# Kernel optimization log

Hardware: AMD Instinct MI355X
Metric: run time of the kernel (lower is better)

The kernel has to match this reference:

```python
import jax, jax.numpy as jnp
import numpy as np

B, V, J, NB = 512, 6890, 24, 10
P = (J - 1) * 9  # 207 pose-blendshape features

# Standard SMPL kinematic tree (root parent = -1)
SMPL_PARENTS = np.array([-1, 0, 0, 0, 1, 2, 3, 4, 5, 6, 7, 8, 9, 9, 9,
                         12, 13, 14, 16, 17, 18, 19, 20, 21], dtype=np.int32)


def setup_inputs() -> dict:
    key = jax.random.key(0)
    ks = jax.random.split(key, 7)
    betas = jax.random.normal(ks[0], (B, NB), jnp.float32)
    pose = 0.2 * jax.random.normal(ks[1], (B, J * 3), jnp.float32)
    v_template = jax.random.normal(ks[2], (V, 3), jnp.float32)
    shapedirs = 0.01 * jax.random.normal(ks[3], (V, 3, NB), jnp.float32)
    posedirs = 0.01 * jax.random.normal(ks[4], (P, V * 3), jnp.float32)
    J_regressor = jax.random.uniform(ks[5], (J, V), jnp.float32)
    J_regressor = J_regressor / jnp.sum(J_regressor, axis=1, keepdims=True)
    lbs_weights = jax.random.uniform(ks[6], (V, J), jnp.float32)
    lbs_weights = lbs_weights / jnp.sum(lbs_weights, axis=1, keepdims=True)
    parents = jnp.asarray(SMPL_PARENTS)
    return {"betas": betas, "pose": pose, "v_template": v_template,
            "shapedirs": shapedirs, "posedirs": posedirs,
            "J_regressor": J_regressor, "lbs_weights": lbs_weights,
            "parents": parents}


def batch_rodrigues(aa):
    """Axis-angle (N,3) -> rotation matrices (N,3,3), matching the torch impl."""
    angle = jnp.linalg.norm(aa + 1e-8, axis=1, keepdims=True)  # (N,1)
    rd = aa / angle
    cos = jnp.cos(angle)[:, :, None]  # (N,1,1)
    sin = jnp.sin(angle)[:, :, None]
    rx, ry, rz = rd[:, 0], rd[:, 1], rd[:, 2]
    zeros = jnp.zeros_like(rx)
    K = jnp.stack([zeros, -rz, ry,
                   rz, zeros, -rx,
                   -ry, rx, zeros], axis=1).reshape(-1, 3, 3)
    ident = jnp.eye(3, dtype=aa.dtype)
    return ident + sin * K + (1.0 - cos) * jnp.matmul(K, K)


def reference(betas, pose, v_template, shapedirs, posedirs, J_regressor,
              lbs_weights, parents):
    par = np.asarray(parents)  # static kinematic tree (host constants)
    b = betas.shape[0]
    nj = J_regressor.shape[0]
    # shape blendshapes: v_shaped = v_template + sum_l betas_l * shapedirs[...,l]
    v_shaped = v_template[None] + jnp.einsum('bl,vkl->bvk', betas, shapedirs)
    Jloc = jnp.einsum('bvk,jv->bjk', v_shaped, J_regressor)  # (b,J,3)
    rot = batch_rodrigues(pose.reshape(-1, 3)).reshape(b, nj, 3, 3)
    # pose blendshapes
    ident = jnp.eye(3, dtype=rot.dtype)
    pose_feature = (rot[:, 1:] - ident).reshape(b, -1)  # (b,207)
    v_posed = v_shaped + (pose_feature @ posedirs).reshape(b, -1, 3)
    # relative joint locations
    rel = Jloc.at[:, 1:].add(-Jloc[:, par[1:]])
    # per-joint local transforms (b,J,4,4)
    top = jnp.concatenate([rot, rel[..., None]], axis=-1)  # (b,J,3,4)
    bottom = jnp.broadcast_to(jnp.array([0., 0., 0., 1.], dtype=rot.dtype),
                              (b, nj, 1, 4))
    tm = jnp.concatenate([top, bottom], axis=2)
    # kinematic chain (fixed, tiny loop over 24 joints with static parents)
    chain = [tm[:, 0]]
    for i in range(1, par.shape[0]):
        chain.append(chain[par[i]] @ tm[:, i])
    transforms = jnp.stack(chain, axis=1)  # (b,J,4,4) absolute transforms
    posed_joints = transforms[:, :, :3, 3]
    # remove rest-pose joint offset: A = transforms - [0|transforms @ [J;0]]
    jh = jnp.concatenate([Jloc, jnp.zeros_like(Jloc[..., :1])], axis=-1)
    init_bone = jnp.einsum('bjpq,bjq->bjp', transforms, jh)  # (b,J,4)
    A = transforms - jnp.pad(init_bone[..., None], ((0, 0), (0, 0), (0, 0), (3, 0)))
    # linear blend skinning: per-vertex transform T = sum_j w_vj * A_j
    T = jnp.einsum('vj,bjpq->bvpq', lbs_weights, A)  # (b,V,4,4)
    verts = jnp.einsum('bvpk,bvk->bvp', T[:, :, :3, :3], v_posed) + T[:, :, :3, 3]
    return verts, posed_joints, A, transforms, v_posed
```

## Files before the change

kernel.cpp:

```cpp
#include <hip/hip_runtime.h>
#include <hip/hip_bf16.h>

#define BB 512
#define VV 6890
#define NJ 24
#define NBETA 10
#define NP 207
#define N3 (VV*3)
#define TBAT 16

#define OFF_VERTS 0
#define OFF_PJ   (BB*VV*3)
#define OFF_A    (OFF_PJ + BB*NJ*3)
#define OFF_TF   (OFF_A + BB*NJ*16)
#define OFF_VP   (OFF_TF + BB*NJ*16)

#define WS_JTJS 0
#define WS_PF   (WS_JTJS + NJ*33)
#define WS_A    (WS_PF + BB*NP)

__constant__ int c_par[NJ] = {-1, 0, 0, 0, 1, 2, 3, 4, 5, 6, 7, 8,
                              9, 9, 9, 12, 13, 14, 16, 17, 18, 19, 20, 21};

__global__ void k_jreg(const float* __restrict__ jr,
                       const float* __restrict__ vt,
                       const float* __restrict__ sd,
                       float* __restrict__ ws) {
    int j = blockIdx.x / 33, idx = blockIdx.x % 33;
    int t = threadIdx.x;
    float acc = 0.f;
    for (int v = t; v < VV; v += 256) {
        float a = jr[j * VV + v];
        float x = (idx < 3) ? vt[v * 3 + idx] : sd[v * 30 + (idx - 3)];
        acc += a * x;
    }
    __shared__ float red[256];
    red[t] = acc;
    __syncthreads();
    for (int s = 128; s > 0; s >>= 1) {
        if (t < s) red[t] += red[t + s];
        __syncthreads();
    }
    if (t == 0) ws[WS_JTJS + j * 33 + idx] = red[0];
}

__global__ __launch_bounds__(64) void k_chain(
        const float* __restrict__ betas,
        const float* __restrict__ pose,
        const float* __restrict__ ws_jtjs,
        float* __restrict__ ws_pf,
        float* __restrict__ ws_A,
        float* __restrict__ out) {
    int b = blockIdx.x;
    int t = threadIdx.x;
    __shared__ float Jl[NJ][3];
    __shared__ float tm[NJ][16];
    __shared__ float ch[NJ][16];
    float R[9];

    if (t < NJ) {
        int j = t;
        float bb[NBETA];
#pragma unroll
        for (int l = 0; l < NBETA; l++) bb[l] = betas[b * NBETA + l];
#pragma unroll
        for (int k = 0; k < 3; k++) {
            float acc = ws_jtjs[j * 33 + k];
#pragma unroll
            for (int l = 0; l < NBETA; l++) acc += bb[l] * ws_jtjs[j * 33 + 3 + k * NBETA + l];
            Jl[j][k] = acc;
        }
        float ax = pose[b * NJ * 3 + j * 3 + 0];
        float ay = pose[b * NJ * 3 + j * 3 + 1];
        float az = pose[b * NJ * 3 + j * 3 + 2];
        float e0 = ax + 1e-8f, e1 = ay + 1e-8f, e2 = az + 1e-8f;
        float ang = sqrtf(e0 * e0 + e1 * e1 + e2 * e2);
        float inv = 1.f / ang;
        float rx = ax * inv, ry = ay * inv, rz = az * inv;
        float sn = sinf(ang), cs = cosf(ang);
        float Km[9] = {0.f, -rz, ry, rz, 0.f, -rx, -ry, rx, 0.f};
#pragma unroll
        for (int r = 0; r < 3; r++)
#pragma unroll
            for (int c = 0; c < 3; c++) {
                float kk = Km[3 * r + 0] * Km[0 + c] + Km[3 * r + 1] * Km[3 + c] +
                           Km[3 * r + 2] * Km[6 + c];
                R[3 * r + c] = ((r == c) ? 1.f : 0.f) + sn * Km[3 * r + c] + (1.f - cs) * kk;
            }
        if (j >= 1) {
#pragma unroll
            for (int e = 0; e < 9; e++) {
                int r = e / 3, c = e % 3;
                ws_pf[b * NP + (j - 1) * 9 + e] = R[e] - ((r == c) ? 1.f : 0.f);
            }
        }
    }
    __syncthreads();
    if (t < NJ) {
        int j = t;
        int p = c_par[j];
        int ps = (p < 0) ? 0 : p;
#pragma unroll
        for (int r = 0; r < 3; r++) {
            tm[j][r * 4 + 0] = R[3 * r + 0];
            tm[j][r * 4 + 1] = R[3 * r + 1];
            tm[j][r * 4 + 2] = R[3 * r + 2];
            tm[j][r * 4 + 3] = (j == 0) ? Jl[j][r] : (Jl[j][r] - Jl[ps][r]);
        }
        tm[j][12] = 0.f; tm[j][13] = 0.f; tm[j][14] = 0.f; tm[j][15] = 1.f;
    }
    __syncthreads();
    if (t < 16) ch[0][t] = tm[0][t];
    __syncthreads();
    for (int i = 1; i < NJ; i++) {
        if (t < 16) {
            int r = t >> 2, c = t & 3;
            int p = c_par[i];
            ch[i][t] = ch[p][4 * r + 0] * tm[i][0 + c] + ch[p][4 * r + 1] * tm[i][4 + c] +
                       ch[p][4 * r + 2] * tm[i][8 + c] + ch[p][4 * r + 3] * tm[i][12 + c];
        }
        __syncthreads();
    }
    if (t < NJ) {
        int j = t;
        float ib[4];
#pragma unroll
        for (int p = 0; p < 4; p++)
            ib[p] = ch[j][4 * p + 0] * Jl[j][0] + ch[j][4 * p + 1] * Jl[j][1] +
                    ch[j][4 * p + 2] * Jl[j][2];
#pragma unroll
        for (int e = 0; e < 16; e++) {
            int r = e >> 2, c = e & 3;
            float tr = ch[j][e];
            float Ae = tr - ((c == 3) ? ib[r] : 0.f);
            out[OFF_TF + (size_t)(b * NJ + j) * 16 + e] = tr;
            out[OFF_A + (size_t)(b * NJ + j) * 16 + e] = Ae;
            ws_A[(size_t)(b * NJ + j) * 16 + e] = Ae;
        }
#pragma unroll
        for (int k = 0; k < 3; k++)
            out[OFF_PJ + (size_t)(b * NJ + j) * 3 + k] = ch[j][4 * k + 3];
    }
}

__global__ __launch_bounds__(256, 4) void k_posed(
        const float* __restrict__ vt,
        const float* __restrict__ sd,
        const float* __restrict__ betas,
        const float* __restrict__ pd,
        const float* __restrict__ ws_pf,
        float* __restrict__ out) {
    int b0 = blockIdx.y * TBAT;
    int n0 = (blockIdx.x * 256 + threadIdx.x) * 2;
    if (n0 >= N3) return;

    float acc0[TBAT], acc1[TBAT];
#pragma unroll
    for (int bi = 0; bi < TBAT; bi++) { acc0[bi] = 0.f; acc1[bi] = 0.f; }

    for (int p0 = 0; p0 < NP; p0 += 9) {
        float pdv0[9], pdv1[9];
#pragma unroll
        for (int pc = 0; pc < 9; pc++) {
            const float2 v = *(const float2*)&pd[(size_t)(p0 + pc) * N3 + n0];
            pdv0[pc] = v.x; pdv1[pc] = v.y;
        }
#pragma unroll
        for (int bi = 0; bi < TBAT; bi++) {
            const float* __restrict__ pfr = &ws_pf[(size_t)(b0 + bi) * NP + p0];
#pragma unroll
            for (int pc = 0; pc < 9; pc++) {
                float w = pfr[pc];
                acc0[bi] += w * pdv0[pc];
                acc1[bi] += w * pdv1[pc];
            }
        }
    }

    float base0 = vt[n0], base1 = vt[n0 + 1];
    float sdv0[NBETA], sdv1[NBETA];
#pragma unroll
    for (int l = 0; l < NBETA; l++) {
        sdv0[l] = sd[(size_t)n0 * NBETA + l];
        sdv1[l] = sd[(size_t)(n0 + 1) * NBETA + l];
    }
#pragma unroll
    for (int bi = 0; bi < TBAT; bi++) {
        const float* __restrict__ br = &betas[(size_t)(b0 + bi) * NBETA];
        float s0 = base0 + acc0[bi], s1 = base1 + acc1[bi];
#pragma unroll
        for (int l = 0; l < NBETA; l++) {
            float bl = br[l];
            s0 += bl * sdv0[l];
            s1 += bl * sdv1[l];
        }
        float2 o; o.x = s0; o.y = s1;
        *(float2*)&out[OFF_VP + (size_t)(b0 + bi) * N3 + n0] = o;
    }
}

__global__ void k_verts(const float* __restrict__ lw,
                        const float* __restrict__ ws_A,
                        float* __restrict__ out) {
    int b = blockIdx.y;
    int v = blockIdx.x * 256 + threadIdx.x;
    if (v >= VV) return;

    float wv[NJ];
#pragma unroll
    for (int j0 = 0; j0 < NJ; j0 += 4) {
        const float4 w4 = *(const float4*)&lw[(size_t)v * NJ + j0];
        wv[j0 + 0] = w4.x; wv[j0 + 1] = w4.y; wv[j0 + 2] = w4.z; wv[j0 + 3] = w4.w;
    }

    float T[12];
#pragma unroll
    for (int e = 0; e < 12; e++) T[e] = 0.f;
    const float* __restrict__ Ab = ws_A + (size_t)b * NJ * 16;
#pragma unroll
    for (int j = 0; j < NJ; j++) {
        const float* __restrict__ Aj = Ab + j * 16;
        float wj = wv[j];
#pragma unroll
        for (int e = 0; e < 12; e++) T[e] += wj * Aj[e];
    }

    size_t base = (size_t)(b * VV + v) * 3;
    float x = out[OFF_VP + base + 0];
    float y = out[OFF_VP + base + 1];
    float z = out[OFF_VP + base + 2];
#pragma unroll
    for (int p = 0; p < 3; p++) {
        out[OFF_VERTS + base + p] =
            T[4 * p + 0] * x + T[4 * p + 1] * y + T[4 * p + 2] * z + T[4 * p + 3];
    }
}

extern "C" void kernel_launch(void* const* d_in, const int* in_sizes, int n_in,
                              void* d_out, int out_size, void* d_ws, size_t ws_size,
                              hipStream_t stream) {
    const float* betas = (const float*)d_in[0];
    const float* pose  = (const float*)d_in[1];
    const float* vt    = (const float*)d_in[2];
    const float* sd    = (const float*)d_in[3];
    const float* pd    = (const float*)d_in[4];
    const float* jr    = (const float*)d_in[5];
    const float* lw    = (const float*)d_in[6];
    float* out = (float*)d_out;
    float* ws = (float*)d_ws;

    k_jreg<<<NJ * 33, 256, 0, stream>>>(jr, vt, sd, ws);
    k_chain<<<BB, 64, 0, stream>>>(betas, pose, ws + WS_JTJS, ws + WS_PF,
                                   ws + WS_A, out);
    k_posed<<<dim3((N3 / 2 + 255) / 256, BB / TBAT), 256, 0, stream>>>(
        vt, sd, betas, pd, ws + WS_PF, out);
    k_verts<<<dim3((VV + 255) / 256, BB), 256, 0, stream>>>(lw, ws + WS_A, out);
}
```

Baseline: 231.0 us.

## Restructure jreg, posed, and verts kernels with chunking, XCD swizzle, and batching

After: 255.4 us. 1.11x slower.

```diff
diff --git a/kernel.cpp b/kernel.cpp
--- a/kernel.cpp
+++ b/kernel.cpp
@@ -7,7 +7,10 @@
 #define NBETA 10
 #define NP 207
 #define N3 (VV*3)
-#define TBAT 16
+#define TBAT 8
+#define NCH 16
+#define CHV ((VV + NCH - 1) / NCH)
+#define VB 4
 
 #define OFF_VERTS 0
 #define OFF_PJ   (BB*VV*3)
@@ -15,39 +18,58 @@
 #define OFF_TF   (OFF_A + BB*NJ*16)
 #define OFF_VP   (OFF_TF + BB*NJ*16)
 
-#define WS_JTJS 0
-#define WS_PF   (WS_JTJS + NJ*33)
+#define WS_JP   0
+#define WS_PF   (WS_JP + NCH*NJ*33)
 #define WS_A    (WS_PF + BB*NP)
 
 __constant__ int c_par[NJ] = {-1, 0, 0, 0, 1, 2, 3, 4, 5, 6, 7, 8,
                               9, 9, 9, 12, 13, 14, 16, 17, 18, 19, 20, 21};
 
-__global__ void k_jreg(const float* __restrict__ jr,
-                       const float* __restrict__ vt,
-                       const float* __restrict__ sd,
-                       float* __restrict__ ws) {
-    int j = blockIdx.x / 33, idx = blockIdx.x % 33;
+__global__ __launch_bounds__(256) void k_jreg(const float* __restrict__ jr,
+                                              const float* __restrict__ vt,
+                                              const float* __restrict__ sd,
+                                              float* __restrict__ ws_jp) {
+    int j = blockIdx.x, ch = blockIdx.y;
     int t = threadIdx.x;
-    float acc = 0.f;
-    for (int v = t; v < VV; v += 256) {
-        float a = jr[j * VV + v];
-        float x = (idx < 3) ? vt[v * 3 + idx] : sd[v * 30 + (idx - 3)];
-        acc += a * x;
-    }
-    __shared__ float red[256];
-    red[t] = acc;
+    int v0 = ch * CHV;
+    int vend = (v0 + CHV < VV) ? (v0 + CHV) : VV;
+
+    float acc[33];
+#pragma unroll
+    for (int i = 0; i < 33; i++) acc[i] = 0.f;
+
+    for (int v = v0 + t; v < vend; v += 256) {
+        float a = jr[(size_t)j * VV + v];
+        acc[0] += a * vt[v * 3 + 0];
+        acc[1] += a * vt[v * 3 + 1];
+        acc[2] += a * vt[v * 3 + 2];
+        const float2* sp = (const float2*)&sd[(size_t)v * 30];
+#pragma unroll
+        for (int i = 0; i < 15; i++) {
+            float2 s = sp[i];
+            acc[3 + 2 * i] += a * s.x;
+            acc[4 + 2 * i] += a * s.y;
+        }
+    }
+
+    __shared__ float red[33][256];
+#pragma unroll
+    for (int i = 0; i < 33; i++) red[i][t] = acc[i];
     __syncthreads();
     for (int s = 128; s > 0; s >>= 1) {
-        if (t < s) red[t] += red[t + s];
+        if (t < s) {
+#pragma unroll
+            for (int i = 0; i < 33; i++) red[i][t] += red[i][t + s];
+        }
         __syncthreads();
     }
-    if (t == 0) ws[WS_JTJS + j * 33 + idx] = red[0];
+    if (t < 33) ws_jp[(size_t)(ch * NJ + j) * 33 + t] = red[t][0];
 }
 
 __global__ __launch_bounds__(64) void k_chain(
         const float* __restrict__ betas,
         const float* __restrict__ pose,
-        const float* __restrict__ ws_jtjs,
+        const float* __restrict__ ws_jp,
         float* __restrict__ ws_pf,
         float* __restrict__ ws_A,
         float* __restrict__ out) {
@@ -60,14 +82,22 @@
 
     if (t < NJ) {
         int j = t;
+        float s[33];
+#pragma unroll
+        for (int i = 0; i < 33; i++) s[i] = 0.f;
+        for (int c = 0; c < NCH; c++) {
+            const float* pp = ws_jp + (size_t)(c * NJ + j) * 33;
+#pragma unroll
+            for (int i = 0; i < 33; i++) s[i] += pp[i];
+        }
         float bb[NBETA];
 #pragma unroll
         for (int l = 0; l < NBETA; l++) bb[l] = betas[b * NBETA + l];
 #pragma unroll
         for (int k = 0; k < 3; k++) {
-            float acc = ws_jtjs[j * 33 + k];
-#pragma unroll
-            for (int l = 0; l < NBETA; l++) acc += bb[l] * ws_jtjs[j * 33 + 3 + k * NBETA + l];
+            float acc = s[k];
+#pragma unroll
+            for (int l = 0; l < NBETA; l++) acc += bb[l] * s[3 + k * NBETA + l];
             Jl[j][k] = acc;
         }
         float ax = pose[b * NJ * 3 + j * 3 + 0];
@@ -143,6 +173,29 @@
     }
 }
 
+__device__ __forceinline__ void load9(const float* __restrict__ pdp, int c0,
+                                      float* b0, float* b1) {
+#pragma unroll
+    for (int pc = 0; pc < 9; pc++) {
+        float2 v = *(const float2*)&pdp[(size_t)(c0 + pc) * N3];
+        b0[pc] = v.x; b1[pc] = v.y;
+    }
+}
+__device__ __forceinline__ void comp9(const float* __restrict__ ws_pf, int b0, int c0,
+                                      const float* pv0, const float* pv1,
+                                      float* acc0, float* acc1) {
+#pragma unroll
+    for (int bi = 0; bi < TBAT; bi++) {
+        const float* __restrict__ pfr = &ws_pf[(size_t)(b0 + bi) * NP + c0];
+#pragma unroll
+        for (int pc = 0; pc < 9; pc++) {
+            float w = pfr[pc];
+            acc0[bi] += w * pv0[pc];
+            acc1[bi] += w * pv1[pc];
+        }
+    }
+}
+
 __global__ __launch_bounds__(256, 4) void k_posed(
         const float* __restrict__ vt,
         const float* __restrict__ sd,
@@ -150,32 +203,33 @@
         const float* __restrict__ pd,
         const float* __restrict__ ws_pf,
         float* __restrict__ out) {
-    int b0 = blockIdx.y * TBAT;
-    int n0 = (blockIdx.x * 256 + threadIdx.x) * 2;
+    int id = blockIdx.x;
+    int xcd = id & 7, li = id >> 3;
+    int nx = (xcd == 0) ? 6 : 5;
+    if (li >= nx * (BB / TBAT)) return;
+    int x = xcd + 8 * (li % nx);
+    int y = li / nx;
+    int b0 = y * TBAT;
+    int n0 = (x * 256 + threadIdx.x) * 2;
     if (n0 >= N3) return;
 
     float acc0[TBAT], acc1[TBAT];
 #pragma unroll
     for (int bi = 0; bi < TBAT; bi++) { acc0[bi] = 0.f; acc1[bi] = 0.f; }
 
-    for (int p0 = 0; p0 < NP; p0 += 9) {
-        float pdv0[9], pdv1[9];
-#pragma unroll
-        for (int pc = 0; pc < 9; pc++) {
-            const float2 v = *(const float2*)&pd[(size_t)(p0 + pc) * N3 + n0];
-            pdv0[pc] = v.x; pdv1[pc] = v.y;
-        }
-#pragma unroll
-        for (int bi = 0; bi < TBAT; bi++) {
-            const float* __restrict__ pfr = &ws_pf[(size_t)(b0 + bi) * NP + p0];
-#pragma unroll
-            for (int pc = 0; pc < 9; pc++) {
-                float w = pfr[pc];
-                acc0[bi] += w * pdv0[pc];
-                acc1[bi] += w * pdv1[pc];
-            }
-        }
-    }
+    float pA0[9], pA1[9], pB0[9], pB1[9];
+    const float* __restrict__ pdp = pd + n0;
+
+    load9(pdp, 0, pA0, pA1);
+#pragma unroll 1
+    for (int c = 0; c < 11; c++) {
+        int c0 = c * 18;
+        load9(pdp, c0 + 9, pB0, pB1);
+        comp9(ws_pf, b0, c0, pA0, pA1, acc0, acc1);
+        load9(pdp, c0 + 18, pA0, pA1);
+        comp9(ws_pf, b0, c0 + 9, pB0, pB1, acc0, acc1);
+    }
+    comp9(ws_pf, b0, 198, pA0, pA1, acc0, acc1);
 
     float base0 = vt[n0], base1 = vt[n0 + 1];
     float sdv0[NBETA], sdv1[NBETA];
@@ -199,10 +253,10 @@
     }
 }
 
-__global__ void k_verts(const float* __restrict__ lw,
-                        const float* __restrict__ ws_A,
-                        float* __restrict__ out) {
-    int b = blockIdx.y;
+__global__ __launch_bounds__(256, 4) void k_verts(const float* __restrict__ lw,
+                                                  const float* __restrict__ ws_A,
+                                                  float* __restrict__ out) {
+    int bq = blockIdx.y;
     int v = blockIdx.x * 256 + threadIdx.x;
     if (v >= VV) return;
 
@@ -213,26 +267,29 @@
         wv[j0 + 0] = w4.x; wv[j0 + 1] = w4.y; wv[j0 + 2] = w4.z; wv[j0 + 3] = w4.w;
     }
 
-    float T[12];
-#pragma unroll
-    for (int e = 0; e < 12; e++) T[e] = 0.f;
-    const float* __restrict__ Ab = ws_A + (size_t)b * NJ * 16;
-#pragma unroll
-    for (int j = 0; j < NJ; j++) {
-        const float* __restrict__ Aj = Ab + j * 16;
-        float wj = wv[j];
-#pragma unroll
-        for (int e = 0; e < 12; e++) T[e] += wj * Aj[e];
-    }
-
-    size_t base = (size_t)(b * VV + v) * 3;
-    float x = out[OFF_VP + base + 0];
-    float y = out[OFF_VP + base + 1];
-    float z = out[OFF_VP + base + 2];
-#pragma unroll
-    for (int p = 0; p < 3; p++) {
-        out[OFF_VERTS + base + p] =
-            T[4 * p + 0] * x + T[4 * p + 1] * y + T[4 * p + 2] * z + T[4 * p + 3];
+#pragma unroll
+    for (int bb = 0; bb < VB; bb++) {
+        int b = bq * VB + bb;
+        const float* __restrict__ Ab = ws_A + (size_t)b * NJ * 16;
+        float T[12];
+#pragma unroll
+        for (int e = 0; e < 12; e++) T[e] = 0.f;
+#pragma unroll
+        for (int j = 0; j < NJ; j++) {
+            const float* __restrict__ Aj = Ab + j * 16;
+            float wj = wv[j];
+#pragma unroll
+            for (int e = 0; e < 12; e++) T[e] += wj * Aj[e];
+        }
+        size_t base = (size_t)(b * VV + v) * 3;
+        float xx = out[OFF_VP + base + 0];
+        float yy = out[OFF_VP + base + 1];
+        float zz = out[OFF_VP + base + 2];
+#pragma unroll
+        for (int p = 0; p < 3; p++) {
+            out[OFF_VERTS + base + p] =
+                T[4 * p + 0] * xx + T[4 * p + 1] * yy + T[4 * p + 2] * zz + T[4 * p + 3];
+        }
     }
 }
 
@@ -249,10 +306,10 @@
     float* out = (float*)d_out;
     float* ws = (float*)d_ws;
 
-    k_jreg<<<NJ * 33, 256, 0, stream>>>(jr, vt, sd, ws);
-    k_chain<<<BB, 64, 0, stream>>>(betas, pose, ws + WS_JTJS, ws + WS_PF,
+    k_jreg<<<dim3(NJ, NCH), 256, 0, stream>>>(jr, vt, sd, ws + WS_JP);
+    k_chain<<<BB, 64, 0, stream>>>(betas, pose, ws + WS_JP, ws + WS_PF,
                                    ws + WS_A, out);
-    k_posed<<<dim3((N3 / 2 + 255) / 256, BB / TBAT), 256, 0, stream>>>(
+    k_posed<<<8 * 6 * (BB / TBAT), 256, 0, stream>>>(
         vt, sd, betas, pd, ws + WS_PF, out);
-    k_verts<<<dim3((VV + 255) / 256, BB), 256, 0, stream>>>(lw, ws + WS_A, out);
-}
+    k_verts<<<dim3((VV + 255) / 256, BB / VB), 256, 0, stream>>>(lw, ws + WS_A, out);
+}
```
